# Kernel optimization log

Measured on AMD Instinct MI355X. Metric: run time of the kernel, lower is better.

The kernel has to match this reference:

```python
import jax, jax.numpy as jnp
import numpy as np
from jax import lax


def _conv2d_same(x, w):
    # x: [B,Cin,H,W], w: [Cout,Cin,kh,kw], stride 1, SAME padding
    return lax.conv_general_dilated(x, w, (1, 1), 'SAME',
                                    dimension_numbers=('NCHW', 'OIHW', 'NCHW'))


def _descriptor(f_flat, w_a, b_a, w_aa, b_aa, w_m, b_m, w_mm, b_mm):
    # f_flat: [B,C,HW]; channel MLPs on avg/max pooled descriptors (1x1 convs == linear)
    avg = jnp.mean(f_flat, axis=-1)  # [B,C]
    mx = jnp.max(f_flat, axis=-1)    # [B,C]
    a = jax.nn.relu(avg @ w_a.T + b_a) @ w_aa.T + b_aa  # [B,C]
    m = jax.nn.relu(mx @ w_m.T + b_m) @ w_mm.T + b_mm   # [B,C]
    return a + m


def _spatial_gate(a_flat, b, c, h, w, conv1_w, conv1_b, conv2_w, conv2_b):
    a = a_flat.reshape(b, c, h, w)
    pooled = jnp.stack([jnp.mean(a, axis=1), jnp.max(a, axis=1)], axis=1)  # [B,2,H,W]
    y = jax.nn.relu(_conv2d_same(pooled, conv1_w) + conv1_b[None, :, None, None])
    y = _conv2d_same(y, conv2_w) + conv2_b[None, :, None, None]
    return jax.nn.softmax(y.reshape(b, 1, h * w), axis=-1)  # [B,1,HW]


def _cafm_forward(f1, f2,
                  w_avg1, b_avg1, w_max1, b_max1, w_avg11, b_avg11, w_max11, b_max11,
                  w_avg2, b_avg2, w_max2, b_max2, w_avg22, b_avg22, w_max22, b_max22,
                  conv1_w, conv1_b, conv2_w, conv2_b):
    b, c, h, w = f1.shape
    f1f = f1.reshape(b, c, h * w)
    f2f = f2.reshape(b, c, h * w)
    a1 = _descriptor(f1f, w_avg1, b_avg1, w_avg11, b_avg11, w_max1, b_max1, w_max11, b_max11)
    a2 = _descriptor(f2f, w_avg2, b_avg2, w_avg22, b_avg22, w_max2, b_max2, w_max22, b_max22)
    cross = jnp.einsum('bi,bj->bij', a1, a2)  # [B,C,C]
    at1 = jnp.einsum('bij,bjn->bin', jax.nn.softmax(cross, axis=-1), f1f)
    at2 = jnp.einsum('bij,bjn->bin', jax.nn.softmax(cross.transpose(0, 2, 1), axis=-1), f2f)
    g1 = _spatial_gate(at1, b, c, h, w, conv1_w, conv1_b, conv2_w, conv2_b)
    g2 = _spatial_gate(at2, b, c, h, w, conv1_w, conv1_b, conv2_w, conv2_b)
    o1 = (f1f * g1 + f1f).reshape(b, c, h, w)
    o2 = (f2f * g2 + f2f).reshape(b, c, h, w)
    return o1, o2


def setup_inputs() -> dict:
    key = jax.random.key(0)
    ks = jax.random.split(key, 24)
    B, C, H, W = 4, 64, 256, 256
    CR = 32  # reduction channels
    s = 0.05
    d = {
        'f1': jax.random.normal(ks[0], (B, C, H, W), jnp.float32),
        'f2': jax.random.normal(ks[1], (B, C, H, W), jnp.float32),
        'w_avg1': jax.random.normal(ks[2], (CR, C), jnp.float32) * s,
        'b_avg1': jnp.zeros((CR,), jnp.float32),
        'w_max1': jax.random.normal(ks[3], (CR, C), jnp.float32) * s,
        'b_max1': jnp.zeros((CR,), jnp.float32),
        'w_avg11': jax.random.normal(ks[4], (C, CR), jnp.float32) * s,
        'b_avg11': jnp.zeros((C,), jnp.float32),
        'w_max11': jax.random.normal(ks[5], (C, CR), jnp.float32) * s,
        'b_max11': jnp.zeros((C,), jnp.float32),
        'w_avg2': jax.random.normal(ks[6], (CR, C), jnp.float32) * s,
        'b_avg2': jnp.zeros((CR,), jnp.float32),
        'w_max2': jax.random.normal(ks[7], (CR, C), jnp.float32) * s,
        'b_max2': jnp.zeros((CR,), jnp.float32),
        'w_avg22': jax.random.normal(ks[8], (C, CR), jnp.float32) * s,
        'b_avg22': jnp.zeros((C,), jnp.float32),
        'w_max22': jax.random.normal(ks[9], (C, CR), jnp.float32) * s,
        'b_max22': jnp.zeros((C,), jnp.float32),
        'conv1_w': jax.random.normal(ks[10], (1, 2, 3, 3), jnp.float32) * s,
        'conv1_b': jnp.zeros((1,), jnp.float32),
        'conv2_w': jax.random.normal(ks[11], (1, 1, 3, 3), jnp.float32) * s,
        'conv2_b': jnp.zeros((1,), jnp.float32),
    }
    return d


def reference(f1, f2,
              w_avg1, b_avg1, w_max1, b_max1, w_avg11, b_avg11, w_max11, b_max11,
              w_avg2, b_avg2, w_max2, b_max2, w_avg22, b_avg22, w_max22, b_max22,
              conv1_w, conv1_b, conv2_w, conv2_b):
    return _cafm_forward(f1, f2,
                         w_avg1, b_avg1, w_max1, b_max1, w_avg11, b_avg11, w_max11, b_max11,
                         w_avg2, b_avg2, w_max2, b_max2, w_avg22, b_avg22, w_max22, b_max22,
                         conv1_w, conv1_b, conv2_w, conv2_b)
```

## Files before the change

### kernel.cpp

```cpp
#include <hip/hip_runtime.h>
#include <hip/hip_bf16.h>
#include <cstdint>

#define HW 65536

typedef __attribute__((ext_vector_type(8))) short bf16x8;
typedef __attribute__((ext_vector_type(4))) float f32x4;

#define D0   0
#define D1A  4096
#define D2   4624
#define D3   8720
#define FLAGS_BYTES 51264
#define OFF_PARTS 12816
#define OFF_PARTM 143888
#define OFF_AVG   274960
#define OFF_MXA   275472
#define OFF_POOL  292368
#define OFF_BM    1340944
#define OFF_BS    1341968
#define OFF_Y     1342992

__device__ __forceinline__ void st_wt_f32(float* p, float v) {
  __hip_atomic_store(p, v, __ATOMIC_RELAXED, __HIP_MEMORY_SCOPE_AGENT);
}
__device__ __forceinline__ void st_wt_u32(unsigned* p, unsigned v) {
  __hip_atomic_store(p, v, __ATOMIC_RELAXED, __HIP_MEMORY_SCOPE_AGENT);
}

__device__ __forceinline__ void signal(unsigned* slot) {
  __syncthreads();
  if (threadIdx.x == 0) {
    asm volatile("s_waitcnt vmcnt(0)" ::: "memory");
    st_wt_u32(slot, 1u);
  }
}

__device__ __forceinline__ void wait_slots(const unsigned* fl, int idx, bool active) {
  bool ok;
  do {
    ok = true;
    if (active)
      ok = (__hip_atomic_load(fl + idx, __ATOMIC_RELAXED, __HIP_MEMORY_SCOPE_AGENT) != 0u);
    if (!ok) __builtin_amdgcn_s_sleep(8);
  } while (__syncthreads_and((int)ok) == 0);
  asm volatile("" ::: "memory");
}

__device__ __forceinline__ void stage_tile(const float* __restrict__ fb, int n0,
                                           unsigned short* tile, int tid) {
  int r0 = tid >> 6, cb = (tid & 63) << 2;
#pragma unroll 4
  for (int i = 0; i < 16; ++i) {
    int row = (i << 2) + r0;
    float4 v = *(const float4*)(fb + (size_t)row * HW + n0 + cb);
    __hip_bfloat162 lo = __float22bfloat162_rn(make_float2(v.x, v.y));
    __hip_bfloat162 hi = __float22bfloat162_rn(make_float2(v.z, v.w));
    unsigned* d = (unsigned*)(tile + row * 258 + cb);
    d[0] = *(unsigned*)&lo;
    d[1] = *(unsigned*)&hi;
  }
}

template <bool STORE>
__device__ __forceinline__ void p0_tile(const float* __restrict__ fb, int n0, int ssp,
                                        int chunk, unsigned short* tile,
                                        float* __restrict__ ws, int lane, int wv) {
  int ls = lane >> 4, lp = lane & 15;
#pragma unroll
  for (int rg = 0; rg < 4; ++rg) {
    int row = (wv << 4) + (rg << 2) + ls;
    const float4* rp = (const float4*)(fb + (size_t)row * HW + n0);
    float sum = 0.f, mx = -3.4e38f;
#pragma unroll
    for (int i = 0; i < 4; ++i) {
      int j = lp + (i << 4);
      float4 v = rp[j];
      sum += (v.x + v.y) + (v.z + v.w);
      mx = fmaxf(mx, fmaxf(fmaxf(v.x, v.y), fmaxf(v.z, v.w)));
      if (STORE) {
        __hip_bfloat162 lo = __float22bfloat162_rn(make_float2(v.x, v.y));
        __hip_bfloat162 hi = __float22bfloat162_rn(make_float2(v.z, v.w));
        unsigned* d = (unsigned*)(tile + row * 258 + (j << 2));
        d[0] = *(unsigned*)&lo;
        d[1] = *(unsigned*)&hi;
      }
    }
#pragma unroll
    for (int o = 1; o < 16; o <<= 1) {
      sum += __shfl_xor(sum, o);
      mx = fmaxf(mx, __shfl_xor(mx, o));
    }
    if (lp == 0) {
      st_wt_f32(ws + OFF_PARTS + (((ssp << 6) + row) << 8) + chunk, sum);
      st_wt_f32(ws + OFF_PARTM + (((ssp << 6) + row) << 8) + chunk, mx);
    }
  }
}

__global__ __launch_bounds__(256, 4) void k_mega(
    const float* __restrict__ f1, const float* __restrict__ f2,
    float* __restrict__ ws, float* __restrict__ out,
    const float* __restrict__ w_avg1, const float* __restrict__ b_avg1,
    const float* __restrict__ w_max1, const float* __restrict__ b_max1,
    const float* __restrict__ w_avg11, const float* __restrict__ b_avg11,
    const float* __restrict__ w_max11, const float* __restrict__ b_max11,
    const float* __restrict__ w_avg2, const float* __restrict__ b_avg2,
    const float* __restrict__ w_max2, const float* __restrict__ b_max2,
    const float* __restrict__ w_avg22, const float* __restrict__ b_avg22,
    const float* __restrict__ w_max22, const float* __restrict__ b_max22,
    const float* __restrict__ cw1, const float* __restrict__ cb1,
    const float* __restrict__ cw2, const float* __restrict__ cb2) {

  __shared__ union {
    unsigned short tile[64 * 258];
    struct { float pl[2][20][36]; float t1l[18][34]; } cv;
    float yst[512];
  } sm;
  __shared__ float red[8];
  __shared__ float s_in[4][64];
  __shared__ float s_h[4][32];
  __shared__ float s_a1[64], s_a2[64], s_mm[4];
  __shared__ float s_rm[2][64], s_ri[2][64];

  unsigned* fl = (unsigned*)ws;
  const int tid = threadIdx.x;
  const int bx  = blockIdx.x;
  const int lane = tid & 63, wv = tid >> 6;

  const int ss1 = bx >> 8, chunk = bx & 255, n0 = chunk << 8;
  const float* fb1 = f1 + ((size_t)ss1 << 22);
  const float* fb2 = f2 + ((size_t)ss1 << 22);

  p0_tile<true >(fb1, n0, ss1,     chunk, sm.tile, ws, lane, wv);
  p0_tile<false>(fb2, n0, ss1 + 4, chunk, sm.tile, ws, lane, wv);
  signal(fl + D0 + (bx << 2));

  if (bx < 128) {
    int ssx = bx >> 4;
    wait_slots(fl, D0 + ((((ssx & 3) << 8) | tid) << 2), true);
    int r = (bx << 2) + wv;
    float4 s4 = *(const float4*)(ws + OFF_PARTS + (r << 8) + (lane << 2));
    float4 m4 = *(const float4*)(ws + OFF_PARTM + (r << 8) + (lane << 2));
    float s = (s4.x + s4.y) + (s4.z + s4.w);
    float m = fmaxf(fmaxf(m4.x, m4.y), fmaxf(m4.z, m4.w));
    for (int o = 32; o > 0; o >>= 1) {
      s += __shfl_xor(s, o);
      m = fmaxf(m, __shfl_xor(m, o));
    }
    if (lane == 0) {
      st_wt_f32(ws + OFF_AVG + r, s * (1.f / 65536.f));
      st_wt_f32(ws + OFF_MXA + r, m);
    }
    signal(fl + D1A + (bx << 2));
  }

  {
    int fidx = (tid < 16) ? (ss1 * 16 + tid) : ((ss1 + 4) * 16 + (tid - 16));
    wait_slots(fl, D1A + (fidx << 2), tid < 32);
  }
  if (tid < 64) {
    s_in[0][tid] = ws[OFF_AVG + (ss1 << 6) + tid];
    s_in[1][tid] = ws[OFF_MXA + (ss1 << 6) + tid];
    s_in[2][tid] = ws[OFF_AVG + ((ss1 + 4) << 6) + tid];
    s_in[3][tid] = ws[OFF_MXA + ((ss1 + 4) << 6) + tid];
  }
  __syncthreads();
  if (tid < 128) {
    int u = tid & 31, which = tid >> 5;
    const float* W = (which == 0) ? w_avg1 : (which == 1) ? w_max1
                   : (which == 2) ? w_avg2 : w_max2;
    const float* B = (which == 0) ? b_avg1 : (which == 1) ? b_max1
                   : (which == 2) ? b_avg2 : b_max2;
    float s = B[u];
    for (int c2 = 0; c2 < 64; ++c2) s += W[u * 64 + c2] * s_in[which][c2];
    s_h[which][u] = fmaxf(s, 0.f);
  }
  __syncthreads();
  if (tid < 128) {
    int u = tid & 63, which = tid >> 6;
    const float* Wa = which ? w_avg22 : w_avg11;
    const float* Wm = which ? w_max22 : w_max11;
    float s = which ? (b_avg22[u] + b_max22[u]) : (b_avg11[u] + b_max11[u]);
    const float* ha = s_h[which ? 2 : 0];
    const float* hm = s_h[which ? 3 : 1];
    for (int k = 0; k < 32; ++k) s += Wa[u * 32 + k] * ha[k] + Wm[u * 32 + k] * hm[k];
    (which ? s_a2 : s_a1)[u] = s;
  }
  __syncthreads();
  if (wv == 0) {
    float v = s_a2[lane], mxv = v, mnv = v;
    for (int o = 32; o > 0; o >>= 1) {
      mxv = fmaxf(mxv, __shfl_xor(mxv, o));
      mnv = fminf(mnv, __shfl_xor(mnv, o));
    }
    if (lane == 0) { s_mm[0] = mxv; s_mm[1] = mnv; }
  } else if (wv == 1) {
    float v = s_a1[lane], mxv = v, mnv = v;
    for (int o = 32; o > 0; o >>= 1) {
      mxv = fmaxf(mxv, __shfl_xor(mxv, o));
      mnv = fminf(mnv, __shfl_xor(mnv, o));
    }
    if (lane == 0) { s_mm[2] = mxv; s_mm[3] = mnv; }
  }
  __syncthreads();
  {
    int r = tid >> 1, half = tid & 1;
    int sel = r >> 6, i = r & 63;
    float sv = sel ? s_a2[i] : s_a1[i];
    const float* col = sel ? s_a1 : s_a2;
    float mrow = (sv >= 0.f) ? sv * (sel ? s_mm[2] : s_mm[0])
                             : sv * (sel ? s_mm[3] : s_mm[1]);
    float sum = 0.f;
    int j0 = half << 5;
    for (int j = j0; j < j0 + 32; ++j) sum += __expf(sv * col[j] - mrow);
    sum += __shfl_xor(sum, 1);
    if (half == 0) { s_rm[sel][i] = mrow; s_ri[sel][i] = 1.f / sum; }
  }
  __syncthreads();

  {
    const int c = lane & 15, q = lane >> 4;
    const int pxb = wv << 6;

    auto build_A = [&](int sel, bf16x8 (&A)[4][2]) {
      const float* col = sel ? s_a1 : s_a2;
#pragma unroll
      for (int mt = 0; mt < 4; ++mt) {
        int i = mt * 16 + c;
        float sv = sel ? s_a2[i] : s_a1[i];
        float mrow = s_rm[sel][i], inv = s_ri[sel][i];
#pragma unroll
        for (int s = 0; s < 2; ++s) {
          union { bf16x8 v; __hip_bfloat162 h[4]; } u;
#pragma unroll
          for (int jj = 0; jj < 4; ++jj) {
            int j = s * 32 + q * 8 + jj * 2;
            float e0 = __expf(sv * col[j]     - mrow) * inv;
            float e1 = __expf(sv * col[j + 1] - mrow) * inv;
            u.h[jj] = __float22bfloat162_rn(make_float2(e0, e1));
          }
          A[mt][s] = u.v;
        }
      }
    };

    auto mfma_tile = [&](int ss, const bf16x8 (&A)[4][2]) {
      float* poolp = ws + OFF_POOL + (size_t)ss * (2 * HW);
#pragma unroll
      for (int nt = 0; nt < 4; ++nt) {
        int pcol = pxb + (nt << 4) + c;
        union { bf16x8 v; unsigned short s[8]; } u0, u1;
#pragma unroll
        for (int j = 0; j < 8; ++j) {
          u0.s[j] = sm.tile[(q * 8 + j) * 258 + pcol];
          u1.s[j] = sm.tile[(32 + q * 8 + j) * 258 + pcol];
        }
        f32x4 acc[4];
#pragma unroll
        for (int mt = 0; mt < 4; ++mt) {
          acc[mt] = (f32x4){0.f, 0.f, 0.f, 0.f};
          acc[mt] = __builtin_amdgcn_mfma_f32_16x16x32_bf16(A[mt][0], u0.v, acc[mt], 0, 0, 0);
          acc[mt] = __builtin_amdgcn_mfma_f32_16x16x32_bf16(A[mt][1], u1.v, acc[mt], 0, 0, 0);
        }
        float sum = 0.f, mxv = -3.4e38f;
#pragma unroll
        for (int mt = 0; mt < 4; ++mt)
#pragma unroll
          for (int r = 0; r < 4; ++r) {
            float v = acc[mt][r];
            sum += v;
            mxv = fmaxf(mxv, v);
          }
        sum += __shfl_xor(sum, 16);
        sum += __shfl_xor(sum, 32);
        mxv = fmaxf(mxv, __shfl_xor(mxv, 16));
        mxv = fmaxf(mxv, __shfl_xor(mxv, 32));
        int px = n0 + pcol;
        if (q == 0) st_wt_f32(poolp + px, sum * (1.f / 64.f));
        if (q == 1) st_wt_f32(poolp + HW + px, mxv);
      }
    };

    bf16x8 A[4][2];
    build_A(0, A);
    mfma_tile(ss1, A);
    __syncthreads();
    stage_tile(fb2, n0, sm.tile, tid);
    __syncthreads();
    build_A(1, A);
    mfma_tile(ss1 + 4, A);
  }
  signal(fl + D2 + (bx << 2));

  {
    int ss = bx >> 7, tile_id = bx & 127;
    int h0 = (tile_id >> 3) << 4;
    int w0 = (tile_id & 7) << 5;
    {
      int rr = h0 - 2 + tid;
      bool act = (tid < 20) && (rr >= 0) && (rr < 256);
      wait_slots(fl, D2 + ((((ss & 3) << 8) + rr) << 2), act);
    }
    const float* pp = ws + OFF_POOL + (size_t)ss * (2 * HW);
    float c1b = cb1[0], c2b = cb2[0];
    for (int i = tid; i < 1440; i += 256) {
      int ch = (i >= 720), rem = i - ch * 720;
      int rr = rem / 36, cc = rem - rr * 36;
      int h = h0 - 2 + rr, w = w0 - 2 + cc;
      float v = 0.f;
      if (h >= 0 && h < 256 && w >= 0 && w < 256) v = pp[ch * HW + (h << 8) + w];
      sm.cv.pl[ch][rr][cc] = v;
    }
    __syncthreads();
    for (int i = tid; i < 612; i += 256) {
      int rr = i / 34, cc = i - rr * 34;
      int h = h0 - 1 + rr, w = w0 - 1 + cc;
      float s = c1b;
#pragma unroll
      for (int ci = 0; ci < 2; ++ci)
#pragma unroll
        for (int kh = 0; kh < 3; ++kh)
#pragma unroll
          for (int kw = 0; kw < 3; ++kw)
            s += sm.cv.pl[ci][rr + kh][cc + kw] * cw1[ci * 9 + kh * 3 + kw];
      bool in = (h >= 0 && h < 256 && w >= 0 && w < 256);
      sm.cv.t1l[rr][cc] = in ? fmaxf(s, 0.f) : 0.f;
    }
    __syncthreads();
    float myy[2];
    float m = -3.4e38f;
#pragma unroll
    for (int k2 = 0; k2 < 2; ++k2) {
      int i = tid + (k2 << 8);
      int rr = i >> 5, cc = i & 31;
      float s = c2b;
#pragma unroll
      for (int kh = 0; kh < 3; ++kh)
#pragma unroll
        for (int kw = 0; kw < 3; ++kw)
          s += sm.cv.t1l[rr + kh][cc + kw] * cw2[kh * 3 + kw];
      st_wt_f32(ws + OFF_Y + (ss << 16) + ((h0 + rr) << 8) + w0 + cc, s);
      myy[k2] = s;
      m = fmaxf(m, s);
    }
    for (int o = 32; o > 0; o >>= 1) m = fmaxf(m, __shfl_xor(m, o));
    if (lane == 0) red[wv] = m;
    __syncthreads();
    float Mb = fmaxf(fmaxf(red[0], red[1]), fmaxf(red[2], red[3]));
    float z = __expf(myy[0] - Mb) + __expf(myy[1] - Mb);
    for (int o = 32; o > 0; o >>= 1) z += __shfl_xor(z, o);
    if (lane == 0) red[4 + wv] = z;
    __syncthreads();
    if (tid == 0) {
      st_wt_f32(ws + OFF_BM + bx, Mb);
      st_wt_f32(ws + OFF_BS + bx, red[4] + red[5] + red[6] + red[7]);
    }
  }
  signal(fl + D3 + (bx << 2));

  {
    int ss = bx >> 7, wq = bx & 127;
    wait_slots(fl, D3 + ((ss * 128 + (tid & 127)) << 2), tid < 128);
    float m = (tid < 128) ? ws[OFF_BM + ss * 128 + tid] : -3.4e38f;
    for (int o = 32; o > 0; o >>= 1) m = fmaxf(m, __shfl_xor(m, o));
    if (lane == 0) red[wv] = m;
    __syncthreads();
    float M = fmaxf(fmaxf(red[0], red[1]), fmaxf(red[2], red[3]));
    float z = (tid < 128) ? __expf(ws[OFF_BM + ss * 128 + tid] - M) * ws[OFF_BS + ss * 128 + tid] : 0.f;
    for (int o = 32; o > 0; o >>= 1) z += __shfl_xor(z, o);
    if (lane == 0) red[4 + wv] = z;
    __syncthreads();
    float iZ = 1.f / (red[4] + red[5] + red[6] + red[7]);
    int p0 = wq << 9;
    if (tid < 128) {
      float4 vy = *(const float4*)(ws + OFF_Y + (ss << 16) + p0 + (tid << 2));
      *(float4*)(&sm.yst[tid << 2]) = vy;
    }
    __syncthreads();
    const float* fsl = (ss >= 4) ? (f2 + ((size_t)(ss - 4) << 22))
                                 : (f1 + ((size_t)ss << 22));
    float* osl = out + ((size_t)ss << 22);
    int c0 = tid >> 7;
    int pxo = (tid & 127) << 2;
    float4 yv = *(const float4*)(&sm.yst[pxo]);
    f32x4 g;
    g.x = 1.f + __expf(yv.x - M) * iZ;
    g.y = 1.f + __expf(yv.y - M) * iZ;
    g.z = 1.f + __expf(yv.z - M) * iZ;
    g.w = 1.f + __expf(yv.w - M) * iZ;
#pragma unroll 8
    for (int i = 0; i < 32; ++i) {
      int ch = (i << 1) + c0;
      size_t gi = (size_t)ch * HW + p0 + pxo;
      f32x4 fv = *(const f32x4*)(fsl + gi);
      f32x4 o = fv * g;
      __builtin_nontemporal_store(o, (f32x4*)(osl + gi));
    }
  }
}

extern "C" void kernel_launch(void* const* d_in, const int* in_sizes, int n_in,
                              void* d_out, int out_size, void* d_ws, size_t ws_size,
                              hipStream_t stream) {
  const float* f1 = (const float*)d_in[0];
  const float* f2 = (const float*)d_in[1];
  const float* w_avg1  = (const float*)d_in[2];
  const float* b_avg1  = (const float*)d_in[3];
  const float* w_max1  = (const float*)d_in[4];
  const float* b_max1  = (const float*)d_in[5];
  const float* w_avg11 = (const float*)d_in[6];
  const float* b_avg11 = (const float*)d_in[7];
  const float* w_max11 = (const float*)d_in[8];
  const float* b_max11 = (const float*)d_in[9];
  const float* w_avg2  = (const float*)d_in[10];
  const float* b_avg2  = (const float*)d_in[11];
  const float* w_max2  = (const float*)d_in[12];
  const float* b_max2  = (const float*)d_in[13];
  const float* w_avg22 = (const float*)d_in[14];
  const float* b_avg22 = (const float*)d_in[15];
  const float* w_max22 = (const float*)d_in[16];
  const float* b_max22 = (const float*)d_in[17];
  const float* conv1_w = (const float*)d_in[18];
  const float* conv1_b = (const float*)d_in[19];
  const float* conv2_w = (const float*)d_in[20];
  const float* conv2_b = (const float*)d_in[21];
  float* ws = (float*)d_ws;
  float* out = (float*)d_out;

  (void)hipMemsetAsync(d_ws, 0, FLAGS_BYTES, stream);
  k_mega<<<1024, 256, 0, stream>>>(f1, f2, ws, out,
                                   w_avg1, b_avg1, w_max1, b_max1,
                                   w_avg11, b_avg11, w_max11, b_max11,
                                   w_avg2, b_avg2, w_max2, b_max2,
                                   w_avg22, b_avg22, w_max22, b_max22,
                                   conv1_w, conv1_b, conv2_w, conv2_b);
}
```

Baseline: 326.0 us.

## Keep f2 tile in registers, pack pooled maps as bf16, prefetch before final wait

The phase-0 pass over f2 now keeps its bf16-converted values in registers, so they no longer have to be re-read from global memory later when the tile is staged into LDS. The pooled mean/max maps are packed into one bf16x2 word per pixel, which halves pool traffic and the conv halo loads. The final phase prefetches the first 8 channel rows of f before spinning on the softmax-stat flags, overlapping that load with the wait. The spin sleep is also shortened. This costs extra registers and reduces pool precision to bf16.

```diff
diff --git a/kernel.cpp b/kernel.cpp
--- a/kernel.cpp
+++ b/kernel.cpp
@@ -42,30 +42,14 @@
     ok = true;
     if (active)
       ok = (__hip_atomic_load(fl + idx, __ATOMIC_RELAXED, __HIP_MEMORY_SCOPE_AGENT) != 0u);
-    if (!ok) __builtin_amdgcn_s_sleep(8);
+    if (!ok) __builtin_amdgcn_s_sleep(4);
   } while (__syncthreads_and((int)ok) == 0);
   asm volatile("" ::: "memory");
 }
 
-__device__ __forceinline__ void stage_tile(const float* __restrict__ fb, int n0,
-                                           unsigned short* tile, int tid) {
-  int r0 = tid >> 6, cb = (tid & 63) << 2;
-#pragma unroll 4
-  for (int i = 0; i < 16; ++i) {
-    int row = (i << 2) + r0;
-    float4 v = *(const float4*)(fb + (size_t)row * HW + n0 + cb);
-    __hip_bfloat162 lo = __float22bfloat162_rn(make_float2(v.x, v.y));
-    __hip_bfloat162 hi = __float22bfloat162_rn(make_float2(v.z, v.w));
-    unsigned* d = (unsigned*)(tile + row * 258 + cb);
-    d[0] = *(unsigned*)&lo;
-    d[1] = *(unsigned*)&hi;
-  }
-}
-
-template <bool STORE>
-__device__ __forceinline__ void p0_tile(const float* __restrict__ fb, int n0, int ssp,
-                                        int chunk, unsigned short* tile,
-                                        float* __restrict__ ws, int lane, int wv) {
+__device__ __forceinline__ void p0_tile_lds(const float* __restrict__ fb, int n0, int ssp,
+                                            int chunk, unsigned short* tile,
+                                            float* __restrict__ ws, int lane, int wv) {
   int ls = lane >> 4, lp = lane & 15;
 #pragma unroll
   for (int rg = 0; rg < 4; ++rg) {
@@ -78,13 +62,43 @@
       float4 v = rp[j];
       sum += (v.x + v.y) + (v.z + v.w);
       mx = fmaxf(mx, fmaxf(fmaxf(v.x, v.y), fmaxf(v.z, v.w)));
-      if (STORE) {
-        __hip_bfloat162 lo = __float22bfloat162_rn(make_float2(v.x, v.y));
-        __hip_bfloat162 hi = __float22bfloat162_rn(make_float2(v.z, v.w));
-        unsigned* d = (unsigned*)(tile + row * 258 + (j << 2));
-        d[0] = *(unsigned*)&lo;
-        d[1] = *(unsigned*)&hi;
-      }
+      __hip_bfloat162 lo = __float22bfloat162_rn(make_float2(v.x, v.y));
+      __hip_bfloat162 hi = __float22bfloat162_rn(make_float2(v.z, v.w));
+      unsigned* d = (unsigned*)(tile + row * 258 + (j << 2));
+      d[0] = *(unsigned*)&lo;
+      d[1] = *(unsigned*)&hi;
+    }
+#pragma unroll
+    for (int o = 1; o < 16; o <<= 1) {
+      sum += __shfl_xor(sum, o);
+      mx = fmaxf(mx, __shfl_xor(mx, o));
+    }
+    if (lp == 0) {
+      st_wt_f32(ws + OFF_PARTS + (((ssp << 6) + row) << 8) + chunk, sum);
+      st_wt_f32(ws + OFF_PARTM + (((ssp << 6) + row) << 8) + chunk, mx);
+    }
+  }
+}
+
+__device__ __forceinline__ void p0_tile_regs(const float* __restrict__ fb, int n0, int ssp,
+                                             int chunk, unsigned (&r2)[16][2],
+                                             float* __restrict__ ws, int lane, int wv) {
+  int ls = lane >> 4, lp = lane & 15;
+#pragma unroll
+  for (int rg = 0; rg < 4; ++rg) {
+    int row = (wv << 4) + (rg << 2) + ls;
+    const float4* rp = (const float4*)(fb + (size_t)row * HW + n0);
+    float sum = 0.f, mx = -3.4e38f;
+#pragma unroll
+    for (int i = 0; i < 4; ++i) {
+      int j = lp + (i << 4);
+      float4 v = rp[j];
+      sum += (v.x + v.y) + (v.z + v.w);
+      mx = fmaxf(mx, fmaxf(fmaxf(v.x, v.y), fmaxf(v.z, v.w)));
+      __hip_bfloat162 lo = __float22bfloat162_rn(make_float2(v.x, v.y));
+      __hip_bfloat162 hi = __float22bfloat162_rn(make_float2(v.z, v.w));
+      r2[rg * 4 + i][0] = *(unsigned*)&lo;
+      r2[rg * 4 + i][1] = *(unsigned*)&hi;
     }
 #pragma unroll
     for (int o = 1; o < 16; o <<= 1) {
@@ -132,8 +146,9 @@
   const float* fb1 = f1 + ((size_t)ss1 << 22);
   const float* fb2 = f2 + ((size_t)ss1 << 22);
 
-  p0_tile<true >(fb1, n0, ss1,     chunk, sm.tile, ws, lane, wv);
-  p0_tile<false>(fb2, n0, ss1 + 4, chunk, sm.tile, ws, lane, wv);
+  unsigned r2[16][2];
+  p0_tile_lds (fb1, n0, ss1,     chunk, sm.tile, ws, lane, wv);
+  p0_tile_regs(fb2, n0, ss1 + 4, chunk, r2,      ws, lane, wv);
   signal(fl + D0 + (bx << 2));
 
   if (bx < 128) {
@@ -246,7 +261,7 @@
     };
 
     auto mfma_tile = [&](int ss, const bf16x8 (&A)[4][2]) {
-      float* poolp = ws + OFF_POOL + (size_t)ss * (2 * HW);
+      unsigned* poolu = (unsigned*)(ws + OFF_POOL) + (size_t)ss * HW;
 #pragma unroll
       for (int nt = 0; nt < 4; ++nt) {
         int pcol = pxb + (nt << 4) + c;
@@ -276,9 +291,8 @@
         sum += __shfl_xor(sum, 32);
         mxv = fmaxf(mxv, __shfl_xor(mxv, 16));
         mxv = fmaxf(mxv, __shfl_xor(mxv, 32));
-        int px = n0 + pcol;
-        if (q == 0) st_wt_f32(poolp + px, sum * (1.f / 64.f));
-        if (q == 1) st_wt_f32(poolp + HW + px, mxv);
+        __hip_bfloat162 pk = __float22bfloat162_rn(make_float2(sum * (1.f / 64.f), mxv));
+        if (q == 0) st_wt_u32(poolu + n0 + pcol, *(unsigned*)&pk);
       }
     };
 
@@ -286,7 +300,20 @@
     build_A(0, A);
     mfma_tile(ss1, A);
     __syncthreads();
-    stage_tile(fb2, n0, sm.tile, tid);
+    {
+      int ls = lane >> 4, lp = lane & 15;
+#pragma unroll
+      for (int rg = 0; rg < 4; ++rg) {
+        int row = (wv << 4) + (rg << 2) + ls;
+#pragma unroll
+        for (int i = 0; i < 4; ++i) {
+          int j = lp + (i << 4);
+          unsigned* d = (unsigned*)(sm.tile + row * 258 + (j << 2));
+          d[0] = r2[rg * 4 + i][0];
+          d[1] = r2[rg * 4 + i][1];
+        }
+      }
+    }
     __syncthreads();
     build_A(1, A);
     mfma_tile(ss1 + 4, A);
@@ -302,15 +329,15 @@
       bool act = (tid < 20) && (rr >= 0) && (rr < 256);
       wait_slots(fl, D2 + ((((ss & 3) << 8) + rr) << 2), act);
     }
-    const float* pp = ws + OFF_POOL + (size_t)ss * (2 * HW);
+    const unsigned* pp = (const unsigned*)(ws + OFF_POOL) + (size_t)ss * HW;
     float c1b = cb1[0], c2b = cb2[0];
-    for (int i = tid; i < 1440; i += 256) {
-      int ch = (i >= 720), rem = i - ch * 720;
-      int rr = rem / 36, cc = rem - rr * 36;
+    for (int i = tid; i < 720; i += 256) {
+      int rr = i / 36, cc = i - rr * 36;
       int h = h0 - 2 + rr, w = w0 - 2 + cc;
-      float v = 0.f;
-      if (h >= 0 && h < 256 && w >= 0 && w < 256) v = pp[ch * HW + (h << 8) + w];
-      sm.cv.pl[ch][rr][cc] = v;
+      unsigned pk = 0u;
+      if (h >= 0 && h < 256 && w >= 0 && w < 256) pk = pp[(h << 8) + w];
+      sm.cv.pl[0][rr][cc] = __uint_as_float(pk << 16);
+      sm.cv.pl[1][rr][cc] = __uint_as_float(pk & 0xffff0000u);
     }
     __syncthreads();
     for (int i = tid; i < 612; i += 256) {
@@ -361,38 +388,48 @@
 
   {
     int ss = bx >> 7, wq = bx & 127;
-    wait_slots(fl, D3 + ((ss * 128 + (tid & 127)) << 2), tid < 128);
-    float m = (tid < 128) ? ws[OFF_BM + ss * 128 + tid] : -3.4e38f;
-    for (int o = 32; o > 0; o >>= 1) m = fmaxf(m, __shfl_xor(m, o));
-    if (lane == 0) red[wv] = m;
-    __syncthreads();
-    float M = fmaxf(fmaxf(red[0], red[1]), fmaxf(red[2], red[3]));
-    float z = (tid < 128) ? __expf(ws[OFF_BM + ss * 128 + tid] - M) * ws[OFF_BS + ss * 128 + tid] : 0.f;
-    for (int o = 32; o > 0; o >>= 1) z += __shfl_xor(z, o);
-    if (lane == 0) red[4 + wv] = z;
-    __syncthreads();
-    float iZ = 1.f / (red[4] + red[5] + red[6] + red[7]);
     int p0 = wq << 9;
-    if (tid < 128) {
-      float4 vy = *(const float4*)(ws + OFF_Y + (ss << 16) + p0 + (tid << 2));
-      *(float4*)(&sm.yst[tid << 2]) = vy;
-    }
-    __syncthreads();
     const float* fsl = (ss >= 4) ? (f2 + ((size_t)(ss - 4) << 22))
                                  : (f1 + ((size_t)ss << 22));
     float* osl = out + ((size_t)ss << 22);
     int c0 = tid >> 7;
     int pxo = (tid & 127) << 2;
+    f32x4 pf[8];
+#pragma unroll
+    for (int i = 0; i < 8; ++i)
+      pf[i] = *(const f32x4*)(fsl + (size_t)((i << 1) + c0) * HW + p0 + pxo);
+
+    wait_slots(fl, D3 + ((ss * 128 + (tid & 127)) << 2), tid < 128);
+    float m = (tid < 128) ? ws[OFF_BM + ss * 128 + tid] : -3.4e38f;
+    for (int o = 32; o > 0; o >>= 1) m = fmaxf(m, __shfl_xor(m, o));
+    if (lane == 0) red[wv] = m;
+    __syncthreads();
+    float M = fmaxf(fmaxf(red[0], red[1]), fmaxf(red[2], red[3]));
+    float z = (tid < 128) ? __expf(ws[OFF_BM + ss * 128 + tid] - M) * ws[OFF_BS + ss * 128 + tid] : 0.f;
+    for (int o = 32; o > 0; o >>= 1) z += __shfl_xor(z, o);
+    if (lane == 0) red[4 + wv] = z;
+    __syncthreads();
+    float iZ = 1.f / (red[4] + red[5] + red[6] + red[7]);
+    if (tid < 128) {
+      float4 vy = *(const float4*)(ws + OFF_Y + (ss << 16) + p0 + (tid << 2));
+      *(float4*)(&sm.yst[tid << 2]) = vy;
+    }
+    __syncthreads();
     float4 yv = *(const float4*)(&sm.yst[pxo]);
     f32x4 g;
     g.x = 1.f + __expf(yv.x - M) * iZ;
     g.y = 1.f + __expf(yv.y - M) * iZ;
     g.z = 1.f + __expf(yv.z - M) * iZ;
     g.w = 1.f + __expf(yv.w - M) * iZ;
+#pragma unroll
+    for (int i = 0; i < 8; ++i) {
+      size_t gi = (size_t)((i << 1) + c0) * HW + p0 + pxo;
+      f32x4 o = pf[i] * g;
+      __builtin_nontemporal_store(o, (f32x4*)(osl + gi));
+    }
 #pragma unroll 8
-    for (int i = 0; i < 32; ++i) {
-      int ch = (i << 1) + c0;
-      size_t gi = (size_t)ch * HW + p0 + pxo;
+    for (int i = 8; i < 32; ++i) {
+      size_t gi = (size_t)((i << 1) + c0) * HW + p0 + pxo;
       f32x4 fv = *(const f32x4*)(fsl + gi);
       f32x4 o = fv * g;
       __builtin_nontemporal_store(o, (f32x4*)(osl + gi));
```

New measurement: 323.3 us. Within noise of the previous version (-0.8%).
